# Optimization experiments

Measured on AMD Instinct MI355X. Metric: run time of the kernel, lower is better.

The kernel has to match this reference:

```python
import jax, jax.numpy as jnp
import numpy as np

THRESHOLD = 8.0
B, C, H, W = 16, 512, 56, 56


def setup_inputs() -> dict:
    key = jax.random.key(0)
    # scale by 3 so per-channel max|x| ~ 13 > threshold -> channels disassemble with T=2
    x = jax.random.normal(key, (B, C, H, W), dtype=jnp.float32) * 3.0
    return {"x": x}


def _plan(x):
    """Host-side plan (mirrors the .item() host sync in the torch module).
    Returns outlier channel ids, the gather index that replicates each outlier
    channel T times, and the matching 1/T scale per output channel."""
    xv = np.asarray(x)
    max_vals = np.max(np.abs(xv), axis=(0, 2, 3))              # [C] per-channel max|x|
    outlier_idx = np.nonzero(max_vals > THRESHOLD)[0]          # channels to disassemble
    T = np.ceil(max_vals[outlier_idx] / THRESHOLD).astype(np.int64)
    rep_idx = np.repeat(outlier_idx, T)                        # each outlier channel repeated T times
    inv_T = np.repeat((1.0 / T).astype(np.float32), T)         # per-output-channel scale 1/T
    return outlier_idx, rep_idx, inv_T


def reference(x):
    outlier_idx, rep_idx, inv_T = _plan(x)
    rep = jnp.asarray(rep_idx)
    scale = jnp.asarray(inv_T)
    # single fused gather + scale replaces the per-channel slice/divide/repeat/concat loop
    disassembled_x = x[:, rep, :, :] * scale[None, :, None, None]
    return disassembled_x, jnp.asarray(outlier_idx)
```

## Files before the change

kernel.cpp:

```cpp
#include <hip/hip_runtime.h>

#define CH    512
#define BATCH 16
#define QB    4
#define NQ    (BATCH / QB)
#define HW    3136
#define HW4   784
#define THRESH 8.0f

typedef float f4 __attribute__((ext_vector_type(4)));

__global__ __launch_bounds__(256) void absmax_kernel(const float* __restrict__ x,
                                                     float* __restrict__ partial) {
    const int c   = blockIdx.x;
    const int q   = blockIdx.y;
    const int tid = threadIdx.x;
    float m = 0.0f;
    for (int bb = 0; bb < QB; ++bb) {
        const int b = q * QB + bb;
        const f4* src = reinterpret_cast<const f4*>(x) + (size_t)(b * CH + c) * HW4;
        for (int p = tid; p < HW4; p += 256) {
            f4 v = src[p];
            m = fmaxf(m, fmaxf(fmaxf(fabsf(v.x), fabsf(v.y)),
                               fmaxf(fabsf(v.z), fabsf(v.w))));
        }
    }
    __shared__ float sm[256];
    sm[tid] = m;
    __syncthreads();
    for (int off = 128; off > 0; off >>= 1) {
        if (tid < off) sm[tid] = fmaxf(sm[tid], sm[tid + off]);
        __syncthreads();
    }
    if (tid == 0) partial[c * NQ + q] = sm[0];
}

__global__ __launch_bounds__(256) void gather_kernel(const float* __restrict__ x,
                                                     const float* __restrict__ partial,
                                                     float* __restrict__ out,
                                                     float* __restrict__ out_tail,
                                                     int R) {
    const int nwg  = gridDim.x;
    const int orig = blockIdx.x;
    const int xcd  = orig & 7;
    const int q8 = nwg >> 3, r8 = nwg & 7;
    const int wg = (xcd < r8 ? xcd * (q8 + 1) : r8 * (q8 + 1) + (xcd - r8) * q8)
                   + (orig >> 3);
    const int j = wg >> 4;
    const int b = wg & 15;

    const int tid  = threadIdx.x;
    const int lane = tid & 63;
    const int w    = tid >> 6;

    const int c0 = tid * 2, c1 = c0 + 1;
    f4 p0 = reinterpret_cast<const f4*>(partial)[tid * 2];
    f4 p1 = reinterpret_cast<const f4*>(partial)[tid * 2 + 1];
    float m0 = fmaxf(fmaxf(p0.x, p0.y), fmaxf(p0.z, p0.w));
    float m1 = fmaxf(fmaxf(p1.x, p1.y), fmaxf(p1.z, p1.w));
    int T0 = (m0 > THRESH) ? (int)ceilf(m0 * 0.125f) : 0;
    int T1 = (m1 > THRESH) ? (int)ceilf(m1 * 0.125f) : 0;
    const int v = T0 + T1;

    int s = v;
    #pragma unroll
    for (int off = 1; off < 64; off <<= 1) {
        int t2 = __shfl_up(s, off, 64);
        if (lane >= off) s += t2;
    }
    __shared__ int wsum[4];
    if (lane == 63) wsum[w] = s;
    __syncthreads();
    int woff = 0;
    #pragma unroll
    for (int k = 0; k < 4; ++k) if (k < w) woff += wsum[k];
    const int excl   = woff + s - v;
    const int start0 = excl, start1 = excl + T0;

    __shared__ int sc, sT;
    if (T0 > 0 && j >= start0 && j < start0 + T0) { sc = c0; sT = T0; }
    if (T1 > 0 && j >= start1 && j < start1 + T1) { sc = c1; sT = T1; }

    if (wg == 0) {
        const int o0 = (T0 > 0), o1 = (T1 > 0);
        const int v2 = o0 + o1;
        int s2 = v2;
        #pragma unroll
        for (int off = 1; off < 64; off <<= 1) {
            int t2 = __shfl_up(s2, off, 64);
            if (lane >= off) s2 += t2;
        }
        __shared__ int wsum2[4];
        if (lane == 63) wsum2[w] = s2;
        __syncthreads();
        int woff2 = 0;
        #pragma unroll
        for (int k = 0; k < 4; ++k) if (k < w) woff2 += wsum2[k];
        const int ex2 = woff2 + s2 - v2;
        if (o0) out_tail[ex2]      = (float)c0;
        if (o1) out_tail[ex2 + o0] = (float)c1;
    }
    __syncthreads();

    const int   c     = sc;
    const float scale = (float)(1.0 / (double)sT);

    const f4* src = reinterpret_cast<const f4*>(x) + (size_t)(b * CH + c) * HW4;
    f4* dst = reinterpret_cast<f4*>(out) + ((size_t)b * R + j) * HW4;
    for (int p = tid; p < HW4; p += 256) {
        f4 vv = src[p];
        vv.x *= scale; vv.y *= scale; vv.z *= scale; vv.w *= scale;
        dst[p] = vv;
    }
}

extern "C" void kernel_launch(void* const* d_in, const int* in_sizes, int n_in,
                              void* d_out, int out_size, void* d_ws, size_t ws_size,
                              hipStream_t stream) {
    const float* x = (const float*)d_in[0];
    float* out = (float*)d_out;

    const int plane = BATCH * HW;
    const int R     = out_size / plane;

    float* partial = (float*)d_ws;

    absmax_kernel<<<dim3(CH, NQ), 256, 0, stream>>>(x, partial);
    if (R > 0) {
        gather_kernel<<<dim3(R * BATCH), 256, 0, stream>>>(
            x, partial, out, out + (size_t)R * plane, R);
    }
}
```

Measured before the change: 69.20 us.

## Restructure gather to one block per source channel, writing all replicas per read

The gather kernel changes from one workgroup per (output channel, batch) to one workgroup per (input channel, batch quarter). Each block reads its source plane once and writes it T times with nontemporal stores, so input reads are no longer repeated for every replica. The XCD-aware block remapping is removed. Non-outlier channels' blocks exit early, and per-block work now varies with T, which can cause load imbalance.

New measurement: 69.38 us. No clear change (+0.3%).

```diff
diff --git a/kernel.cpp b/kernel.cpp
--- a/kernel.cpp
+++ b/kernel.cpp
@@ -40,22 +40,17 @@
                                                      float* __restrict__ out,
                                                      float* __restrict__ out_tail,
                                                      int R) {
-    const int nwg  = gridDim.x;
-    const int orig = blockIdx.x;
-    const int xcd  = orig & 7;
-    const int q8 = nwg >> 3, r8 = nwg & 7;
-    const int wg = (xcd < r8 ? xcd * (q8 + 1) : r8 * (q8 + 1) + (xcd - r8) * q8)
-                   + (orig >> 3);
-    const int j = wg >> 4;
-    const int b = wg & 15;
+    const int w  = blockIdx.x;
+    const int c  = w & (CH - 1);
+    const int bq = w >> 9;
 
     const int tid  = threadIdx.x;
     const int lane = tid & 63;
-    const int w    = tid >> 6;
+    const int wv   = tid >> 6;
 
     const int c0 = tid * 2, c1 = c0 + 1;
-    f4 p0 = reinterpret_cast<const f4*>(partial)[tid * 2];
-    f4 p1 = reinterpret_cast<const f4*>(partial)[tid * 2 + 1];
+    f4 p0 = reinterpret_cast<const f4*>(partial)[c0];
+    f4 p1 = reinterpret_cast<const f4*>(partial)[c1];
     float m0 = fmaxf(fmaxf(p0.x, p0.y), fmaxf(p0.z, p0.w));
     float m1 = fmaxf(fmaxf(p1.x, p1.y), fmaxf(p1.z, p1.w));
     int T0 = (m0 > THRESH) ? (int)ceilf(m0 * 0.125f) : 0;
@@ -69,19 +64,20 @@
         if (lane >= off) s += t2;
     }
     __shared__ int wsum[4];
-    if (lane == 63) wsum[w] = s;
+    if (lane == 63) wsum[wv] = s;
     __syncthreads();
     int woff = 0;
     #pragma unroll
-    for (int k = 0; k < 4; ++k) if (k < w) woff += wsum[k];
-    const int excl   = woff + s - v;
-    const int start0 = excl, start1 = excl + T0;
+    for (int k = 0; k < 4; ++k) if (k < wv) woff += wsum[k];
+    const int start0 = woff + s - v;
+    const int start1 = start0 + T0;
 
-    __shared__ int sc, sT;
-    if (T0 > 0 && j >= start0 && j < start0 + T0) { sc = c0; sT = T0; }
-    if (T1 > 0 && j >= start1 && j < start1 + T1) { sc = c1; sT = T1; }
+    __shared__ short sStart[CH];
+    __shared__ char  sT[CH];
+    sStart[c0] = (short)start0;  sT[c0] = (char)T0;
+    sStart[c1] = (short)start1;  sT[c1] = (char)T1;
 
-    if (wg == 0) {
+    if (w == 0) {
         const int o0 = (T0 > 0), o1 = (T1 > 0);
         const int v2 = o0 + o1;
         int s2 = v2;
@@ -91,26 +87,34 @@
             if (lane >= off) s2 += t2;
         }
         __shared__ int wsum2[4];
-        if (lane == 63) wsum2[w] = s2;
+        if (lane == 63) wsum2[wv] = s2;
         __syncthreads();
         int woff2 = 0;
         #pragma unroll
-        for (int k = 0; k < 4; ++k) if (k < w) woff2 += wsum2[k];
+        for (int k = 0; k < 4; ++k) if (k < wv) woff2 += wsum2[k];
         const int ex2 = woff2 + s2 - v2;
         if (o0) out_tail[ex2]      = (float)c0;
         if (o1) out_tail[ex2 + o0] = (float)c1;
     }
     __syncthreads();
 
-    const int   c     = sc;
-    const float scale = (float)(1.0 / (double)sT);
+    const int T     = sT[c];
+    const int start = sStart[c];
+    if (T == 0) return;
+    const float scale = (float)(1.0 / (double)T);
 
-    const f4* src = reinterpret_cast<const f4*>(x) + (size_t)(b * CH + c) * HW4;
-    f4* dst = reinterpret_cast<f4*>(out) + ((size_t)b * R + j) * HW4;
-    for (int p = tid; p < HW4; p += 256) {
-        f4 vv = src[p];
-        vv.x *= scale; vv.y *= scale; vv.z *= scale; vv.w *= scale;
-        dst[p] = vv;
+    for (int bb = 0; bb < QB; ++bb) {
+        const int b = bq * QB + bb;
+        const f4* src  = reinterpret_cast<const f4*>(x)
+                         + (size_t)(b * CH + c) * HW4;
+        f4*       dst0 = reinterpret_cast<f4*>(out)
+                         + ((size_t)b * R + start) * HW4;
+        for (int p = tid; p < HW4; p += 256) {
+            f4 vv = src[p];
+            vv.x *= scale; vv.y *= scale; vv.z *= scale; vv.w *= scale;
+            for (int k = 0; k < T; ++k)
+                __builtin_nontemporal_store(vv, &dst0[(size_t)k * HW4 + p]);
+        }
     }
 }
 
@@ -127,7 +131,7 @@
 
     absmax_kernel<<<dim3(CH, NQ), 256, 0, stream>>>(x, partial);
     if (R > 0) {
-        gather_kernel<<<dim3(R * BATCH), 256, 0, stream>>>(
+        gather_kernel<<<dim3(CH * NQ), 256, 0, stream>>>(
             x, partial, out, out + (size_t)R * plane, R);
     }
 }
```
